# Kernel optimization log

Hardware: AMD Instinct MI355X
Metric: run time of the kernel (lower is better)

## Reference

```python
import jax, jax.numpy as jnp
import numpy as np

B, T, D = 8, 2048, 1024
H, N = 8, 32  # n_heads, n_state


def _xavier(key, shape, fan_in, fan_out):
    lim = float(np.sqrt(6.0 / (fan_in + fan_out)))
    return jax.random.uniform(key, shape, jnp.float32, -lim, lim)


def setup_inputs() -> dict:
    key = jax.random.key(0)
    ks = jax.random.split(key, 8)
    x = jax.random.normal(ks[0], (B, T, D), jnp.float32)
    W_in = _xavier(ks[1], (D, D), D, D)                    # in_proj.weight [d_inner, dim]
    # per-head xavier on [n_state, d_inner] slices -> limit sqrt(6/(N+D))
    W_k = _xavier(ks[2], (H * N, D), N, D)
    W_v = _xavier(ks[3], (H * N, D), N, D)
    W_q = _xavier(ks[4], (H * N, D), N, D)
    W_beta = _xavier(ks[5], (H * N, D), N, D)
    b_beta = jnp.full((H, N), 2.0, jnp.float32)            # init_beta_bias
    W_out = _xavier(ks[6], (D, H * N), H * N, D)           # out_proj.weight [dim, H*n]
    return {"x": x, "W_in": W_in, "W_k": W_k, "W_v": W_v, "W_q": W_q,
            "W_beta": W_beta, "b_beta": b_beta, "W_out": W_out}


def reference(x, W_in, W_k, W_v, W_q, W_beta, b_beta, W_out):
    b, t, d = x.shape
    h, n = b_beta.shape
    # in_proj + SiLU (use_conv=False)
    xp = jax.nn.silu(jnp.einsum('btd,ed->bte', x, W_in))   # [B,T,D_inner]
    def proj(W):  # -> [T,B,H,N]
        return jnp.einsum('btd,md->btm', xp, W).reshape(b, t, h, n).transpose(1, 0, 2, 3)
    k_all = proj(W_k)
    v_all = proj(W_v)
    q_all = proj(W_q)
    beta_all = jax.nn.sigmoid(proj(W_beta) + b_beta)       # [T,B,H,N]

    S0 = jnp.zeros((b, h, n, n), x.dtype)

    def step(S, inp):
        k, v, q, beta = inp                                 # each [B,H,N]
        kn = k / (jnp.linalg.norm(k, axis=-1, keepdims=True) + 1e-6)
        retrieved = jnp.einsum('bhij,bhj->bhi', S, kn)
        delta = v - retrieved
        S = jnp.tanh(beta[..., None] * S + delta[..., None] * kn[..., None, :])
        Sq = jnp.einsum('bhij,bhj->bhi', S, q)
        out = Sq * jax.nn.silu(Sq)                          # [B,H,N]
        return S, out

    S_final, outs = jax.lax.scan(step, S0, (k_all, v_all, q_all, beta_all))
    cell_out = outs.transpose(1, 0, 2, 3).reshape(b, t, h * n)  # [B,T,H*N]
    y = jnp.einsum('btm,dm->btd', cell_out, W_out)          # out_proj, no bias
    return y, S_final
```

## Files before the change

### kernel.cpp

```cpp
#include <hip/hip_runtime.h>
#include <hip/hip_bf16.h>

#define TT 2048
#define BB 8
#define HH 8
#define NNS 32
#define MM (BB * TT)
#define CH 16

typedef __attribute__((ext_vector_type(8))) short short8;
typedef __attribute__((ext_vector_type(4))) float f32x4;

__device__ __forceinline__ float bf2f(ushort u) {
    return __uint_as_float(((unsigned)u) << 16);
}
__device__ __forceinline__ ushort f2bf(float f) {
    unsigned x = __float_as_uint(f);
    unsigned r = (x + 0x7fffu + ((x >> 16) & 1u)) >> 16;
    return (ushort)r;
}
__device__ __forceinline__ float sigmoidf_fast(float x) {
    float e = __builtin_amdgcn_exp2f(x * -1.4426950408889634f);
    return __builtin_amdgcn_rcpf(1.0f + e);
}
__device__ __forceinline__ float tanhf_fast(float x) {
    float e = __builtin_amdgcn_exp2f(x * 2.8853900817779268f);
    return fmaf(-2.0f, __builtin_amdgcn_rcpf(e + 1.0f), 1.0f);
}

template<int CTRL>
__device__ __forceinline__ float dpp_add(float x) {
    int y = __builtin_amdgcn_update_dpp(0, __float_as_int(x), CTRL, 0xF, 0xF, true);
    return x + __int_as_float(y);
}
__device__ __forceinline__ float red16(float x) {
    x = dpp_add<0xB1>(x);
    x = dpp_add<0x4E>(x);
    x = dpp_add<0x124>(x);
    x = dpp_add<0x128>(x);
    return x;
}

__device__ __forceinline__ void stage8_split(const float* __restrict__ src,
                                             ushort* __restrict__ hi,
                                             ushort* __restrict__ lo) {
    float4 x0 = *reinterpret_cast<const float4*>(src);
    float4 x1 = *reinterpret_cast<const float4*>(src + 4);
    float xs[8] = {x0.x, x0.y, x0.z, x0.w, x1.x, x1.y, x1.z, x1.w};
    ushort h[8], l[8];
#pragma unroll
    for (int i = 0; i < 8; ++i) {
        ushort hh = f2bf(xs[i]);
        h[i] = hh;
        l[i] = f2bf(xs[i] - bf2f(hh));
    }
    *reinterpret_cast<uint4*>(hi) = *reinterpret_cast<const uint4*>(h);
    *reinterpret_cast<uint4*>(lo) = *reinterpret_cast<const uint4*>(l);
}
__device__ __forceinline__ void stage8_hi(const float* __restrict__ src,
                                          ushort* __restrict__ hi) {
    float4 x0 = *reinterpret_cast<const float4*>(src);
    float4 x1 = *reinterpret_cast<const float4*>(src + 4);
    float xs[8] = {x0.x, x0.y, x0.z, x0.w, x1.x, x1.y, x1.z, x1.w};
    ushort h[8];
#pragma unroll
    for (int i = 0; i < 8; ++i) h[i] = f2bf(xs[i]);
    *reinterpret_cast<uint4*>(hi) = *reinterpret_cast<const uint4*>(h);
}

template<int ACT>
__global__ __launch_bounds__(256) void gemm_split(
    const float* __restrict__ A,
    const float* __restrict__ W0, const float* __restrict__ W1,
    const float* __restrict__ W2, const float* __restrict__ W3,
    const float* __restrict__ bbeta,
    float* __restrict__ C, int M, int N, int K)
{
    __shared__ __align__(16) ushort Ah[128][40], Al[128][40];
    __shared__ __align__(16) ushort Wh[128][40], Wl[128][40];
    const int n0 = blockIdx.x * 128;
    const int m0 = blockIdx.y * 128;
    const int t  = threadIdx.x;
    const int wave = t >> 6, lane = t & 63;
    const int lr = lane & 15, lq = lane >> 4;
    const int wm = wave >> 1, wn = wave & 1;

    const float* Wsel;
    {
        int wi = n0 >> 8;
        Wsel = (wi == 0) ? W0 : (wi == 1) ? W1 : (wi == 2) ? W2 : W3;
    }
    const int wr0 = n0 & 255;
    const int sr = t >> 1;
    const int sc = (t & 1) * 16;

    f32x4 acc[4][4];
#pragma unroll
    for (int mi = 0; mi < 4; ++mi)
#pragma unroll
        for (int ni = 0; ni < 4; ++ni) acc[mi][ni] = (f32x4){0.f, 0.f, 0.f, 0.f};

    for (int k0 = 0; k0 < K; k0 += 32) {
        __syncthreads();
        {
            const float* as = &A[(size_t)(m0 + sr) * K + k0 + sc];
            stage8_split(as,     &Ah[sr][sc],     &Al[sr][sc]);
            stage8_split(as + 8, &Ah[sr][sc + 8], &Al[sr][sc + 8]);
            const float* ws = &Wsel[(size_t)(wr0 + sr) * K + k0 + sc];
            stage8_split(ws,     &Wh[sr][sc],     &Wl[sr][sc]);
            stage8_split(ws + 8, &Wh[sr][sc + 8], &Wl[sr][sc + 8]);
        }
        __syncthreads();
        short8 ah[4], al[4], wh[4], wl[4];
#pragma unroll
        for (int mi = 0; mi < 4; ++mi) {
            ah[mi] = *reinterpret_cast<const short8*>(&Ah[wm * 64 + mi * 16 + lr][lq * 8]);
            al[mi] = *reinterpret_cast<const short8*>(&Al[wm * 64 + mi * 16 + lr][lq * 8]);
        }
#pragma unroll
        for (int ni = 0; ni < 4; ++ni) {
            wh[ni] = *reinterpret_cast<const short8*>(&Wh[wn * 64 + ni * 16 + lr][lq * 8]);
            wl[ni] = *reinterpret_cast<const short8*>(&Wl[wn * 64 + ni * 16 + lr][lq * 8]);
        }
#pragma unroll
        for (int mi = 0; mi < 4; ++mi) {
#pragma unroll
            for (int ni = 0; ni < 4; ++ni) {
                acc[mi][ni] = __builtin_amdgcn_mfma_f32_16x16x32_bf16(ah[mi], wh[ni], acc[mi][ni], 0, 0, 0);
                acc[mi][ni] = __builtin_amdgcn_mfma_f32_16x16x32_bf16(ah[mi], wl[ni], acc[mi][ni], 0, 0, 0);
                acc[mi][ni] = __builtin_amdgcn_mfma_f32_16x16x32_bf16(al[mi], wh[ni], acc[mi][ni], 0, 0, 0);
            }
        }
    }

#pragma unroll
    for (int mi = 0; mi < 4; ++mi) {
#pragma unroll
        for (int ni = 0; ni < 4; ++ni) {
#pragma unroll
            for (int r2 = 0; r2 < 4; ++r2) {
                int mg = m0 + wm * 64 + mi * 16 + lq * 4 + r2;
                int ng = n0 + wn * 64 + ni * 16 + lr;
                float v = acc[mi][ni][r2];
                if (ACT == 1) v = v * sigmoidf_fast(v);
                if (ACT == 2 && ng >= 768) v = sigmoidf_fast(v + bbeta[ng - 768]);
                C[(size_t)mg * N + ng] = v;
            }
        }
    }
}

__global__ __launch_bounds__(256) void gemm_bf_a(
    const ushort* __restrict__ A,
    const float* __restrict__ W0, const float* __restrict__ W1,
    const float* __restrict__ W2, const float* __restrict__ W3,
    float* __restrict__ C, int M, int N, int K)
{
    __shared__ __align__(16) ushort As[128][40];
    __shared__ __align__(16) ushort Ws[128][40];
    const int n0 = blockIdx.x * 128;
    const int m0 = blockIdx.y * 128;
    const int t  = threadIdx.x;
    const int wave = t >> 6, lane = t & 63;
    const int lr = lane & 15, lq = lane >> 4;
    const int wm = wave >> 1, wn = wave & 1;

    const float* Wsel;
    {
        int wi = n0 >> 8;
        Wsel = (wi == 0) ? W0 : (wi == 1) ? W1 : (wi == 2) ? W2 : W3;
    }
    const int wr0 = n0 & 255;
    const int sr = t >> 1;
    const int sc = (t & 1) * 16;

    f32x4 acc[4][4];
#pragma unroll
    for (int mi = 0; mi < 4; ++mi)
#pragma unroll
        for (int ni = 0; ni < 4; ++ni) acc[mi][ni] = (f32x4){0.f, 0.f, 0.f, 0.f};

    for (int k0 = 0; k0 < K; k0 += 32) {
        __syncthreads();
        {
            const ushort* as = &A[(size_t)(m0 + sr) * K + k0 + sc];
            *reinterpret_cast<uint4*>(&As[sr][sc])     = *reinterpret_cast<const uint4*>(as);
            *reinterpret_cast<uint4*>(&As[sr][sc + 8]) = *reinterpret_cast<const uint4*>(as + 8);
            const float* ws = &Wsel[(size_t)(wr0 + sr) * K + k0 + sc];
            stage8_hi(ws,     &Ws[sr][sc]);
            stage8_hi(ws + 8, &Ws[sr][sc + 8]);
        }
        __syncthreads();
        short8 af[4], wf[4];
#pragma unroll
        for (int mi = 0; mi < 4; ++mi)
            af[mi] = *reinterpret_cast<const short8*>(&As[wm * 64 + mi * 16 + lr][lq * 8]);
#pragma unroll
        for (int ni = 0; ni < 4; ++ni)
            wf[ni] = *reinterpret_cast<const short8*>(&Ws[wn * 64 + ni * 16 + lr][lq * 8]);
#pragma unroll
        for (int mi = 0; mi < 4; ++mi)
#pragma unroll
            for (int ni = 0; ni < 4; ++ni)
                acc[mi][ni] = __builtin_amdgcn_mfma_f32_16x16x32_bf16(af[mi], wf[ni], acc[mi][ni], 0, 0, 0);
    }

#pragma unroll
    for (int mi = 0; mi < 4; ++mi) {
#pragma unroll
        for (int ni = 0; ni < 4; ++ni) {
#pragma unroll
            for (int r2 = 0; r2 < 4; ++r2) {
                int mg = m0 + wm * 64 + mi * 16 + lq * 4 + r2;
                int ng = n0 + wn * 64 + ni * 16 + lr;
                C[(size_t)mg * N + ng] = acc[mi][ni][r2];
            }
        }
    }
}

__global__ __launch_bounds__(256) void kn_kernel(
    const float* __restrict__ P, float* __restrict__ KN)
{
    int idx = blockIdx.x * 256 + threadIdx.x;
    int col = idx & 255;
    int bt  = idx >> 8;
    float k = P[(size_t)bt * 1024 + col];
    float ks = k * k;
    ks += __shfl_xor(ks, 1, 32);  ks += __shfl_xor(ks, 2, 32);
    ks += __shfl_xor(ks, 4, 32);  ks += __shfl_xor(ks, 8, 32);
    ks += __shfl_xor(ks, 16, 32);
    KN[idx] = k * __builtin_amdgcn_rcpf(sqrtf(ks) + 1e-6f);
}

__device__ __forceinline__ void lds_load8(
    float (&K_)[CH][32], float (&Q_)[CH][32], float (&VB)[CH][8],
    int base, int l, int iw,
    float (&k0)[8], float (&k1)[8], float (&q0)[8], float (&q1)[8],
    float (&vv)[8], float (&bb)[8])
{
#pragma unroll
    for (int u = 0; u < 8; ++u) {
        k0[u] = K_[base + u][l];  k1[u] = K_[base + u][l + 16];
        q0[u] = Q_[base + u][l];  q1[u] = Q_[base + u][l + 16];
        vv[u] = VB[base + u][iw]; bb[u] = VB[base + u][iw + 4];
    }
}

__device__ __forceinline__ void steps8(
    float (&k0)[8], float (&k1)[8], float (&q0)[8], float (&q1)[8],
    float (&vv)[8], float (&bb)[8],
    float& S0, float& S1, float (&sqp)[8])
{
#pragma unroll
    for (int u = 0; u < 8; ++u) {
        float p = red16(fmaf(S0, k0[u], S1 * k1[u]));
        float delta = vv[u] - p;
        S0 = tanhf_fast(fmaf(bb[u], S0, delta * k0[u]));
        S1 = tanhf_fast(fmaf(bb[u], S1, delta * k1[u]));
        sqp[u] = fmaf(S0, q0[u], S1 * q1[u]);
    }
}

__device__ __forceinline__ void flush8(
    float (&sqp)[8], ushort* __restrict__ cell, size_t crow, int l)
{
    float r0 = red16(sqp[0]), r1 = red16(sqp[1]);
    float r2 = red16(sqp[2]), r3 = red16(sqp[3]);
    float r4 = red16(sqp[4]), r5 = red16(sqp[5]);
    float r6 = red16(sqp[6]), r7 = red16(sqp[7]);
    if (l < 8) {
        float s01 = (l & 1) ? r1 : r0;
        float s23 = (l & 1) ? r3 : r2;
        float s45 = (l & 1) ? r5 : r4;
        float s67 = (l & 1) ? r7 : r6;
        float a03 = (l & 2) ? s23 : s01;
        float a47 = (l & 2) ? s67 : s45;
        float sel = (l & 4) ? a47 : a03;
        float o = sel * sel * sigmoidf_fast(sel);
        cell[crow + (size_t)l * 256] = f2bf(o);
    }
}

template<int DO_STAGE>
__device__ __forceinline__ void scan_chunk16(
    float (&K_)[CH][32], float (&Q_)[CH][32], float (&VB)[CH][8],
    float (&NK)[CH][32], float (&NQ)[CH][32], float (&NVB)[CH][8],
    const float*& gkn, const float*& gq, const float*& gv, const float*& gb,
    float (&k0A)[8], float (&k1A)[8], float (&q0A)[8], float (&q1A)[8],
    float (&vvA)[8], float (&bbA)[8],
    float (&k0B)[8], float (&k1B)[8], float (&q0B)[8], float (&q1B)[8],
    float (&vvB)[8], float (&bbB)[8],
    float& S0, float& S1, float (&sqp)[8],
    ushort* __restrict__ cell, size_t crow, int l, int iw, int j)
{
    float4 Lk0, Lk1, Lq0, Lq1;
    float Lv = 0.f, Lb = 0.f;
    if (DO_STAGE) {
        Lk0 = *reinterpret_cast<const float4*>(gkn);
        Lk1 = *reinterpret_cast<const float4*>(gkn + 8 * 256);
        Lq0 = *reinterpret_cast<const float4*>(gq);
        Lq1 = *reinterpret_cast<const float4*>(gq + 8 * 1024);
        Lv  = *gv;
        Lb  = *gb;
        gkn += CH * 256; gq += CH * 1024; gv += CH * 1024; gb += CH * 1024;
    }
    lds_load8(K_, Q_, VB, 8, l, iw, k0B, k1B, q0B, q1B, vvB, bbB);
    steps8(k0A, k1A, q0A, q1A, vvA, bbA, S0, S1, sqp);
    flush8(sqp, cell, crow, l);
    if (DO_STAGE) {
        *reinterpret_cast<float4*>(&NK[j >> 3][(j & 7) * 4]) = Lk0;
        *reinterpret_cast<float4*>(&NK[8 + (j >> 3)][(j & 7) * 4]) = Lk1;
        *reinterpret_cast<float4*>(&NQ[j >> 3][(j & 7) * 4]) = Lq0;
        *reinterpret_cast<float4*>(&NQ[8 + (j >> 3)][(j & 7) * 4]) = Lq1;
        NVB[j >> 2][j & 3] = Lv;
        NVB[j >> 2][4 + (j & 3)] = Lb;
        lds_load8(NK, NQ, NVB, 0, l, iw, k0A, k1A, q0A, q1A, vvA, bbA);
    }
    steps8(k0B, k1B, q0B, q1B, vvB, bbB, S0, S1, sqp);
    flush8(sqp, cell, crow + (size_t)8 * 256, l);
}

__global__ __launch_bounds__(64, 1) void scan_kernel(
    const float* __restrict__ P,
    const float* __restrict__ KN,
    ushort* __restrict__ cell,
    float* __restrict__ Sout)
{
    const int b    = blockIdx.x & 7;
    const int r    = blockIdx.x >> 3;
    const int h    = r & 7;
    const int quad = r >> 3;
    const int j    = threadIdx.x;
    const int l    = j & 15;
    const int iw   = j >> 4;
    const int i    = quad * 4 + iw;

    __shared__ __align__(16) float sK0[CH][32], sK1[CH][32];
    __shared__ __align__(16) float sQ0[CH][32], sQ1[CH][32];
    __shared__ __align__(16) float sVB0[CH][8], sVB1[CH][8];

    const size_t bt0 = (size_t)b * TT;
    const float* gkn = KN + (bt0 + (j >> 3)) * 256 + h * 32 + (j & 7) * 4;
    const float* gq  = P  + (bt0 + (j >> 3)) * 1024 + 512 + h * 32 + (j & 7) * 4;
    const float* gv  = P  + (bt0 + (j >> 2)) * 1024 + 256 + h * 32 + quad * 4 + (j & 3);
    const float* gb  = P  + (bt0 + (j >> 2)) * 1024 + 768 + h * 32 + quad * 4 + (j & 3);

    float k0A[8], k1A[8], q0A[8], q1A[8], vvA[8], bbA[8];
    float k0B[8], k1B[8], q0B[8], q1B[8], vvB[8], bbB[8];
    float sqp[8];
    float S0 = 0.f, S1 = 0.f;
    const size_t cb = (size_t)b * TT * 256 + h * 32 + i;

    {
        float4 K0v = *reinterpret_cast<const float4*>(gkn);
        float4 K1v = *reinterpret_cast<const float4*>(gkn + 8 * 256);
        float4 Q0v = *reinterpret_cast<const float4*>(gq);
        float4 Q1v = *reinterpret_cast<const float4*>(gq + 8 * 1024);
        float v0 = *gv, b0 = *gb;
        gkn += CH * 256; gq += CH * 1024; gv += CH * 1024; gb += CH * 1024;
        *reinterpret_cast<float4*>(&sK0[j >> 3][(j & 7) * 4]) = K0v;
        *reinterpret_cast<float4*>(&sK0[8 + (j >> 3)][(j & 7) * 4]) = K1v;
        *reinterpret_cast<float4*>(&sQ0[j >> 3][(j & 7) * 4]) = Q0v;
        *reinterpret_cast<float4*>(&sQ0[8 + (j >> 3)][(j & 7) * 4]) = Q1v;
        sVB0[j >> 2][j & 3] = v0;
        sVB0[j >> 2][4 + (j & 3)] = b0;
    }
    lds_load8(sK0, sQ0, sVB0, 0, l, iw, k0A, k1A, q0A, q1A, vvA, bbA);

    size_t crow = cb;
    for (int c = 0; c < 63; ++c) {
        scan_chunk16<1>(sK0, sQ0, sVB0, sK1, sQ1, sVB1,
                        gkn, gq, gv, gb,
                        k0A, k1A, q0A, q1A, vvA, bbA,
                        k0B, k1B, q0B, q1B, vvB, bbB,
                        S0, S1, sqp, cell, crow, l, iw, j);
        crow += (size_t)CH * 256;
        scan_chunk16<1>(sK1, sQ1, sVB1, sK0, sQ0, sVB0,
                        gkn, gq, gv, gb,
                        k0A, k1A, q0A, q1A, vvA, bbA,
                        k0B, k1B, q0B, q1B, vvB, bbB,
                        S0, S1, sqp, cell, crow, l, iw, j);
        crow += (size_t)CH * 256;
    }
    scan_chunk16<1>(sK0, sQ0, sVB0, sK1, sQ1, sVB1,
                    gkn, gq, gv, gb,
                    k0A, k1A, q0A, q1A, vvA, bbA,
                    k0B, k1B, q0B, q1B, vvB, bbB,
                    S0, S1, sqp, cell, crow, l, iw, j);
    crow += (size_t)CH * 256;
    scan_chunk16<0>(sK1, sQ1, sVB1, sK0, sQ0, sVB0,
                    gkn, gq, gv, gb,
                    k0A, k1A, q0A, q1A, vvA, bbA,
                    k0B, k1B, q0B, q1B, vvB, bbB,
                    S0, S1, sqp, cell, crow, l, iw, j);

    float* so = Sout + (((size_t)(b * HH + h)) * NNS + i) * NNS;
    so[l] = S0;
    so[l + 16] = S1;
}

extern "C" void kernel_launch(void* const* d_in, const int* in_sizes, int n_in,
                              void* d_out, int out_size, void* d_ws, size_t ws_size,
                              hipStream_t stream) {
    const float* x     = (const float*)d_in[0];
    const float* W_in  = (const float*)d_in[1];
    const float* W_k   = (const float*)d_in[2];
    const float* W_v   = (const float*)d_in[3];
    const float* W_q   = (const float*)d_in[4];
    const float* W_b   = (const float*)d_in[5];
    const float* b_b   = (const float*)d_in[6];
    const float* W_out = (const float*)d_in[7];
    float* out = (float*)d_out;

    const int M = MM;
    float*  xp   = (float*)d_ws;
    float*  P    = xp + (size_t)M * 1024;
    float*  KN   = P  + (size_t)M * 1024;
    ushort* cell = (ushort*)(KN + (size_t)M * 256);

    dim3 blk(256);
    dim3 g1(1024 / 128, M / 128);

    gemm_split<1><<<g1, blk, 0, stream>>>(x, W_in, W_in + 256 * 1024,
                                          W_in + 512 * 1024, W_in + 768 * 1024,
                                          b_b, xp, M, 1024, 1024);
    gemm_split<2><<<g1, blk, 0, stream>>>(xp, W_k, W_v, W_q, W_b,
                                          b_b, P, M, 1024, 1024);
    kn_kernel<<<dim3((M * 256) / 256), blk, 0, stream>>>(P, KN);
    scan_kernel<<<dim3(512), dim3(64), 0, stream>>>(P, KN, cell, out + (size_t)M * 1024);
    gemm_bf_a<<<g1, blk, 0, stream>>>(cell, W_out, W_out + 256 * 256,
                                      W_out + 512 * 256, W_out + 768 * 256,
                                      out, M, 1024, 256);
}
```

Baseline: 639.0 us.

## Pre-split inputs and weights into bf16 planes and double-buffer GEMM tiles

Adds conversion kernels that split x and all weights into bf16 hi/lo planes once, instead of re-splitting fp32 data inside every GEMM tile. The first GEMM now emits its SiLU output directly as bf16 hi/lo planes. The GEMMs load bf16 directly, prefetch the next K-slice into registers, double-buffer shared memory and request two blocks per CU. This cuts redundant conversion work and global fp32 traffic, at the cost of extra conversion passes and workspace.

```diff
diff --git a/kernel.cpp b/kernel.cpp
--- a/kernel.cpp
+++ b/kernel.cpp
@@ -41,43 +41,70 @@
     return x;
 }
 
-__device__ __forceinline__ void stage8_split(const float* __restrict__ src,
-                                             ushort* __restrict__ hi,
-                                             ushort* __restrict__ lo) {
-    float4 x0 = *reinterpret_cast<const float4*>(src);
-    float4 x1 = *reinterpret_cast<const float4*>(src + 4);
+__device__ __forceinline__ void split8(const float4& x0, const float4& x1,
+                                       ushort* __restrict__ h, ushort* __restrict__ l) {
     float xs[8] = {x0.x, x0.y, x0.z, x0.w, x1.x, x1.y, x1.z, x1.w};
-    ushort h[8], l[8];
 #pragma unroll
     for (int i = 0; i < 8; ++i) {
         ushort hh = f2bf(xs[i]);
         h[i] = hh;
         l[i] = f2bf(xs[i] - bf2f(hh));
     }
-    *reinterpret_cast<uint4*>(hi) = *reinterpret_cast<const uint4*>(h);
-    *reinterpret_cast<uint4*>(lo) = *reinterpret_cast<const uint4*>(l);
-}
-__device__ __forceinline__ void stage8_hi(const float* __restrict__ src,
-                                          ushort* __restrict__ hi) {
-    float4 x0 = *reinterpret_cast<const float4*>(src);
-    float4 x1 = *reinterpret_cast<const float4*>(src + 4);
-    float xs[8] = {x0.x, x0.y, x0.z, x0.w, x1.x, x1.y, x1.z, x1.w};
-    ushort h[8];
-#pragma unroll
-    for (int i = 0; i < 8; ++i) h[i] = f2bf(xs[i]);
-    *reinterpret_cast<uint4*>(hi) = *reinterpret_cast<const uint4*>(h);
+}
+
+__global__ __launch_bounds__(256) void conv_x_kernel(
+    const float* __restrict__ src, ushort* __restrict__ hi, ushort* __restrict__ lo)
+{
+    size_t e = ((size_t)blockIdx.x * 256 + threadIdx.x) * 8;
+    float4 x0 = *reinterpret_cast<const float4*>(src + e);
+    float4 x1 = *reinterpret_cast<const float4*>(src + e + 4);
+    ushort h[8], l[8];
+    split8(x0, x1, h, l);
+    *reinterpret_cast<uint4*>(hi + e) = *reinterpret_cast<const uint4*>(h);
+    *reinterpret_cast<uint4*>(lo + e) = *reinterpret_cast<const uint4*>(l);
+}
+
+__global__ __launch_bounds__(256) void conv_w_kernel(
+    const float* __restrict__ Wi, const float* __restrict__ Wk,
+    const float* __restrict__ Wv, const float* __restrict__ Wq,
+    const float* __restrict__ Wb, const float* __restrict__ Wo,
+    ushort* __restrict__ W1h, ushort* __restrict__ W1l,
+    ushort* __restrict__ W2h, ushort* __restrict__ W2l,
+    ushort* __restrict__ W3h)
+{
+    size_t e = ((size_t)blockIdx.x * 256 + threadIdx.x) * 8;
+    const float* s;
+    ushort* dh; ushort* dl; size_t doff; bool dolo = true;
+    if (e < 1048576) {
+        s = Wi + e; dh = W1h; dl = W1l; doff = e;
+    } else if (e < 2097152) {
+        size_t u = e - 1048576;
+        int wi = (int)(u >> 18);
+        const float* sp = (wi == 0) ? Wk : (wi == 1) ? Wv : (wi == 2) ? Wq : Wb;
+        s = sp + (u & 262143); dh = W2h; dl = W2l; doff = u;
+    } else {
+        size_t u = e - 2097152;
+        s = Wo + u; dh = W3h; dl = nullptr; doff = u; dolo = false;
+    }
+    float4 x0 = *reinterpret_cast<const float4*>(s);
+    float4 x1 = *reinterpret_cast<const float4*>(s + 4);
+    ushort h[8], l[8];
+    split8(x0, x1, h, l);
+    *reinterpret_cast<uint4*>(dh + doff) = *reinterpret_cast<const uint4*>(h);
+    if (dolo)
+        *reinterpret_cast<uint4*>(dl + doff) = *reinterpret_cast<const uint4*>(l);
 }
 
 template<int ACT>
-__global__ __launch_bounds__(256) void gemm_split(
-    const float* __restrict__ A,
-    const float* __restrict__ W0, const float* __restrict__ W1,
-    const float* __restrict__ W2, const float* __restrict__ W3,
+__global__ __launch_bounds__(256, 2) void gemm_planes(
+    const ushort* __restrict__ Ah_g, const ushort* __restrict__ Al_g,
+    const ushort* __restrict__ Wh_g, const ushort* __restrict__ Wl_g,
     const float* __restrict__ bbeta,
-    float* __restrict__ C, int M, int N, int K)
-{
-    __shared__ __align__(16) ushort Ah[128][40], Al[128][40];
-    __shared__ __align__(16) ushort Wh[128][40], Wl[128][40];
+    ushort* __restrict__ Ch, ushort* __restrict__ Cl,
+    float* __restrict__ Cf, int M, int N, int K)
+{
+    __shared__ __align__(16) ushort sAh[2][128][40], sAl[2][128][40];
+    __shared__ __align__(16) ushort sWh[2][128][40], sWl[2][128][40];
     const int n0 = blockIdx.x * 128;
     const int m0 = blockIdx.y * 128;
     const int t  = threadIdx.x;
@@ -85,42 +112,67 @@
     const int lr = lane & 15, lq = lane >> 4;
     const int wm = wave >> 1, wn = wave & 1;
 
-    const float* Wsel;
-    {
-        int wi = n0 >> 8;
-        Wsel = (wi == 0) ? W0 : (wi == 1) ? W1 : (wi == 2) ? W2 : W3;
-    }
-    const int wr0 = n0 & 255;
     const int sr = t >> 1;
     const int sc = (t & 1) * 16;
 
+    const ushort* pAh = Ah_g + (size_t)(m0 + sr) * K + sc;
+    const ushort* pAl = Al_g + (size_t)(m0 + sr) * K + sc;
+    const ushort* pWh = Wh_g + (size_t)(n0 + sr) * K + sc;
+    const ushort* pWl = Wl_g + (size_t)(n0 + sr) * K + sc;
+
     f32x4 acc[4][4];
 #pragma unroll
     for (int mi = 0; mi < 4; ++mi)
 #pragma unroll
         for (int ni = 0; ni < 4; ++ni) acc[mi][ni] = (f32x4){0.f, 0.f, 0.f, 0.f};
 
-    for (int k0 = 0; k0 < K; k0 += 32) {
-        __syncthreads();
-        {
-            const float* as = &A[(size_t)(m0 + sr) * K + k0 + sc];
-            stage8_split(as,     &Ah[sr][sc],     &Al[sr][sc]);
-            stage8_split(as + 8, &Ah[sr][sc + 8], &Al[sr][sc + 8]);
-            const float* ws = &Wsel[(size_t)(wr0 + sr) * K + k0 + sc];
-            stage8_split(ws,     &Wh[sr][sc],     &Wl[sr][sc]);
-            stage8_split(ws + 8, &Wh[sr][sc + 8], &Wl[sr][sc + 8]);
-        }
-        __syncthreads();
+    const int NK = K >> 5;
+
+    {
+        uint4 a0 = *reinterpret_cast<const uint4*>(pAh);
+        uint4 a1 = *reinterpret_cast<const uint4*>(pAh + 8);
+        uint4 l0 = *reinterpret_cast<const uint4*>(pAl);
+        uint4 l1 = *reinterpret_cast<const uint4*>(pAl + 8);
+        uint4 w0 = *reinterpret_cast<const uint4*>(pWh);
+        uint4 w1 = *reinterpret_cast<const uint4*>(pWh + 8);
+        uint4 u0 = *reinterpret_cast<const uint4*>(pWl);
+        uint4 u1 = *reinterpret_cast<const uint4*>(pWl + 8);
+        *reinterpret_cast<uint4*>(&sAh[0][sr][sc])     = a0;
+        *reinterpret_cast<uint4*>(&sAh[0][sr][sc + 8]) = a1;
+        *reinterpret_cast<uint4*>(&sAl[0][sr][sc])     = l0;
+        *reinterpret_cast<uint4*>(&sAl[0][sr][sc + 8]) = l1;
+        *reinterpret_cast<uint4*>(&sWh[0][sr][sc])     = w0;
+        *reinterpret_cast<uint4*>(&sWh[0][sr][sc + 8]) = w1;
+        *reinterpret_cast<uint4*>(&sWl[0][sr][sc])     = u0;
+        *reinterpret_cast<uint4*>(&sWl[0][sr][sc + 8]) = u1;
+    }
+    __syncthreads();
+
+    for (int ks = 0; ks < NK; ++ks) {
+        const int cur = ks & 1;
+        uint4 a0, a1, l0, l1, w0, w1, u0, u1;
+        const bool pf = (ks + 1 < NK);
+        if (pf) {
+            const int off = (ks + 1) << 5;
+            a0 = *reinterpret_cast<const uint4*>(pAh + off);
+            a1 = *reinterpret_cast<const uint4*>(pAh + off + 8);
+            l0 = *reinterpret_cast<const uint4*>(pAl + off);
+            l1 = *reinterpret_cast<const uint4*>(pAl + off + 8);
+            w0 = *reinterpret_cast<const uint4*>(pWh + off);
+            w1 = *reinterpret_cast<const uint4*>(pWh + off + 8);
+            u0 = *reinterpret_cast<const uint4*>(pWl + off);
+            u1 = *reinterpret_cast<const uint4*>(pWl + off + 8);
+        }
         short8 ah[4], al[4], wh[4], wl[4];
 #pragma unroll
         for (int mi = 0; mi < 4; ++mi) {
-            ah[mi] = *reinterpret_cast<const short8*>(&Ah[wm * 64 + mi * 16 + lr][lq * 8]);
-            al[mi] = *reinterpret_cast<const short8*>(&Al[wm * 64 + mi * 16 + lr][lq * 8]);
+            ah[mi] = *reinterpret_cast<const short8*>(&sAh[cur][wm * 64 + mi * 16 + lr][lq * 8]);
+            al[mi] = *reinterpret_cast<const short8*>(&sAl[cur][wm * 64 + mi * 16 + lr][lq * 8]);
         }
 #pragma unroll
         for (int ni = 0; ni < 4; ++ni) {
-            wh[ni] = *reinterpret_cast<const short8*>(&Wh[wn * 64 + ni * 16 + lr][lq * 8]);
-            wl[ni] = *reinterpret_cast<const short8*>(&Wl[wn * 64 + ni * 16 + lr][lq * 8]);
+            wh[ni] = *reinterpret_cast<const short8*>(&sWh[cur][wn * 64 + ni * 16 + lr][lq * 8]);
+            wl[ni] = *reinterpret_cast<const short8*>(&sWl[cur][wn * 64 + ni * 16 + lr][lq * 8]);
         }
 #pragma unroll
         for (int mi = 0; mi < 4; ++mi) {
@@ -131,6 +183,18 @@
                 acc[mi][ni] = __builtin_amdgcn_mfma_f32_16x16x32_bf16(al[mi], wh[ni], acc[mi][ni], 0, 0, 0);
             }
         }
+        if (pf) {
+            const int nxt = cur ^ 1;
+            *reinterpret_cast<uint4*>(&sAh[nxt][sr][sc])     = a0;
+            *reinterpret_cast<uint4*>(&sAh[nxt][sr][sc + 8]) = a1;
+            *reinterpret_cast<uint4*>(&sAl[nxt][sr][sc])     = l0;
+            *reinterpret_cast<uint4*>(&sAl[nxt][sr][sc + 8]) = l1;
+            *reinterpret_cast<uint4*>(&sWh[nxt][sr][sc])     = w0;
+            *reinterpret_cast<uint4*>(&sWh[nxt][sr][sc + 8]) = w1;
+            *reinterpret_cast<uint4*>(&sWl[nxt][sr][sc])     = u0;
+            *reinterpret_cast<uint4*>(&sWl[nxt][sr][sc + 8]) = u1;
+        }
+        __syncthreads();
     }
 
 #pragma unroll
@@ -142,67 +206,89 @@
                 int mg = m0 + wm * 64 + mi * 16 + lq * 4 + r2;
                 int ng = n0 + wn * 64 + ni * 16 + lr;
                 float v = acc[mi][ni][r2];
-                if (ACT == 1) v = v * sigmoidf_fast(v);
-                if (ACT == 2 && ng >= 768) v = sigmoidf_fast(v + bbeta[ng - 768]);
-                C[(size_t)mg * N + ng] = v;
+                if (ACT == 1) {
+                    v = v * sigmoidf_fast(v);
+                    ushort h = f2bf(v);
+                    ushort lo_ = f2bf(v - bf2f(h));
+                    Ch[(size_t)mg * N + ng] = h;
+                    Cl[(size_t)mg * N + ng] = lo_;
+                } else {
+                    if (ACT == 2 && ng >= 768) v = sigmoidf_fast(v + bbeta[ng - 768]);
+                    Cf[(size_t)mg * N + ng] = v;
+                }
             }
         }
     }
 }
 
-__global__ __launch_bounds__(256) void gemm_bf_a(
-    const ushort* __restrict__ A,
-    const float* __restrict__ W0, const float* __restrict__ W1,
-    const float* __restrict__ W2, const float* __restrict__ W3,
+__global__ __launch_bounds__(256, 2) void gemm_cell(
+    const ushort* __restrict__ A, const ushort* __restrict__ Wh_g,
     float* __restrict__ C, int M, int N, int K)
 {
-    __shared__ __align__(16) ushort As[128][40];
-    __shared__ __align__(16) ushort Ws[128][40];
+    __shared__ __align__(16) ushort sA[2][128][40];
+    __shared__ __align__(16) ushort sW[2][128][40];
     const int n0 = blockIdx.x * 128;
     const int m0 = blockIdx.y * 128;
     const int t  = threadIdx.x;
     const int wave = t >> 6, lane = t & 63;
     const int lr = lane & 15, lq = lane >> 4;
     const int wm = wave >> 1, wn = wave & 1;
-
-    const float* Wsel;
-    {
-        int wi = n0 >> 8;
-        Wsel = (wi == 0) ? W0 : (wi == 1) ? W1 : (wi == 2) ? W2 : W3;
-    }
-    const int wr0 = n0 & 255;
     const int sr = t >> 1;
     const int sc = (t & 1) * 16;
 
+    const ushort* pA = A    + (size_t)(m0 + sr) * K + sc;
+    const ushort* pW = Wh_g + (size_t)(n0 + sr) * K + sc;
+
     f32x4 acc[4][4];
 #pragma unroll
     for (int mi = 0; mi < 4; ++mi)
 #pragma unroll
         for (int ni = 0; ni < 4; ++ni) acc[mi][ni] = (f32x4){0.f, 0.f, 0.f, 0.f};
 
-    for (int k0 = 0; k0 < K; k0 += 32) {
-        __syncthreads();
-        {
-            const ushort* as = &A[(size_t)(m0 + sr) * K + k0 + sc];
-            *reinterpret_cast<uint4*>(&As[sr][sc])     = *reinterpret_cast<const uint4*>(as);
-            *reinterpret_cast<uint4*>(&As[sr][sc + 8]) = *reinterpret_cast<const uint4*>(as + 8);
-            const float* ws = &Wsel[(size_t)(wr0 + sr) * K + k0 + sc];
-            stage8_hi(ws,     &Ws[sr][sc]);
-            stage8_hi(ws + 8, &Ws[sr][sc + 8]);
-        }
-        __syncthreads();
+    const int NK = K >> 5;
+    {
+        uint4 a0 = *reinterpret_cast<const uint4*>(pA);
+        uint4 a1 = *reinterpret_cast<const uint4*>(pA + 8);
+        uint4 w0 = *reinterpret_cast<const uint4*>(pW);
+        uint4 w1 = *reinterpret_cast<const uint4*>(pW + 8);
+        *reinterpret_cast<uint4*>(&sA[0][sr][sc])     = a0;
+        *reinterpret_cast<uint4*>(&sA[0][sr][sc + 8]) = a1;
+        *reinterpret_cast<uint4*>(&sW[0][sr][sc])     = w0;
+        *reinterpret_cast<uint4*>(&sW[0][sr][sc + 8]) = w1;
+    }
+    __syncthreads();
+
+    for (int ks = 0; ks < NK; ++ks) {
+        const int cur = ks & 1;
+        uint4 a0, a1, w0, w1;
+        const bool pf = (ks + 1 < NK);
+        if (pf) {
+            const int off = (ks + 1) << 5;
+            a0 = *reinterpret_cast<const uint4*>(pA + off);
+            a1 = *reinterpret_cast<const uint4*>(pA + off + 8);
+            w0 = *reinterpret_cast<const uint4*>(pW + off);
+            w1 = *reinterpret_cast<const uint4*>(pW + off + 8);
+        }
         short8 af[4], wf[4];
 #pragma unroll
         for (int mi = 0; mi < 4; ++mi)
-            af[mi] = *reinterpret_cast<const short8*>(&As[wm * 64 + mi * 16 + lr][lq * 8]);
+            af[mi] = *reinterpret_cast<const short8*>(&sA[cur][wm * 64 + mi * 16 + lr][lq * 8]);
 #pragma unroll
         for (int ni = 0; ni < 4; ++ni)
-            wf[ni] = *reinterpret_cast<const short8*>(&Ws[wn * 64 + ni * 16 + lr][lq * 8]);
+            wf[ni] = *reinterpret_cast<const short8*>(&sW[cur][wn * 64 + ni * 16 + lr][lq * 8]);
 #pragma unroll
         for (int mi = 0; mi < 4; ++mi)
 #pragma unroll
             for (int ni = 0; ni < 4; ++ni)
                 acc[mi][ni] = __builtin_amdgcn_mfma_f32_16x16x32_bf16(af[mi], wf[ni], acc[mi][ni], 0, 0, 0);
+        if (pf) {
+            const int nxt = cur ^ 1;
+            *reinterpret_cast<uint4*>(&sA[nxt][sr][sc])     = a0;
+            *reinterpret_cast<uint4*>(&sA[nxt][sr][sc + 8]) = a1;
+            *reinterpret_cast<uint4*>(&sW[nxt][sr][sc])     = w0;
+            *reinterpret_cast<uint4*>(&sW[nxt][sr][sc + 8]) = w1;
+        }
+        __syncthreads();
     }
 
 #pragma unroll
@@ -414,22 +500,32 @@
     float* out = (float*)d_out;
 
     const int M = MM;
-    float*  xp   = (float*)d_ws;
-    float*  P    = xp + (size_t)M * 1024;
-    float*  KN   = P  + (size_t)M * 1024;
+    float* f = (float*)d_ws;
+    float*  P    = f;
+    ushort* Xh   = (ushort*)f;
+    ushort* Xl   = Xh + (size_t)M * 1024;
+    ushort* xpH  = (ushort*)(f + (size_t)M * 1024);
+    ushort* xpL  = xpH + (size_t)M * 1024;
+    float*  KN   = f + (size_t)2 * M * 1024;
     ushort* cell = (ushort*)(KN + (size_t)M * 256);
+    ushort* wb   = cell + (size_t)M * 256;
+    ushort* W1h = wb;
+    ushort* W1l = W1h + 1048576;
+    ushort* W2h = W1l + 1048576;
+    ushort* W2l = W2h + 1048576;
+    ushort* W3h = W2l + 1048576;
 
     dim3 blk(256);
     dim3 g1(1024 / 128, M / 128);
 
-    gemm_split<1><<<g1, blk, 0, stream>>>(x, W_in, W_in + 256 * 1024,
-                                          W_in + 512 * 1024, W_in + 768 * 1024,
-                                          b_b, xp, M, 1024, 1024);
-    gemm_split<2><<<g1, blk, 0, stream>>>(xp, W_k, W_v, W_q, W_b,
-                                          b_b, P, M, 1024, 1024);
+    conv_x_kernel<<<dim3((M * 1024) / (8 * 256)), blk, 0, stream>>>(x, Xh, Xl);
+    conv_w_kernel<<<dim3(2359296 / (8 * 256)), blk, 0, stream>>>(
+        W_in, W_k, W_v, W_q, W_b, W_out, W1h, W1l, W2h, W2l, W3h);
+    gemm_planes<1><<<g1, blk, 0, stream>>>(Xh, Xl, W1h, W1l, b_b,
+                                           xpH, xpL, nullptr, M, 1024, 1024);
+    gemm_planes<2><<<g1, blk, 0, stream>>>(xpH, xpL, W2h, W2l, b_b,
+                                           nullptr, nullptr, P, M, 1024, 1024);
     kn_kernel<<<dim3((M * 256) / 256), blk, 0, stream>>>(P, KN);
     scan_kernel<<<dim3(512), dim3(64), 0, stream>>>(P, KN, cell, out + (size_t)M * 1024);
-    gemm_bf_a<<<g1, blk, 0, stream>>>(cell, W_out, W_out + 256 * 256,
-                                      W_out + 512 * 256, W_out + 768 * 256,
-                                      out, M, 1024, 256);
-}
+    gemm_cell<<<g1, blk, 0, stream>>>(cell, W3h, out, M, 1024, 256);
+}
```

New measurement: 593.7 us. 7.1% less time.
